# Kernel optimization log

Hardware: AMD Instinct MI355X
Metric: run time of the kernel (lower is better)

The kernel has to match this reference:

```python
import jax, jax.numpy as jnp
import numpy as np

B, S, D = 4, 2048, 1024
H = 16
HD = D // H
DFF = 4096
MAX_REL = 32
EPS = 1e-5


def _rms_norm(x, w):
    rms = jnp.sqrt(jnp.mean(x * x, axis=-1, keepdims=True) + EPS)
    return x / rms * w


def setup_inputs() -> dict:
    key = jax.random.key(0)
    ks = jax.random.split(key, 16)
    sc = 0.02
    d = {
        "x": jax.random.normal(ks[0], (B, S, D), dtype=jnp.float32),
        "g1": jnp.ones((D,), dtype=jnp.float32),
        "g2": jnp.ones((D,), dtype=jnp.float32),
        "wq": jax.random.normal(ks[1], (D, D), dtype=jnp.float32) * sc,
        "bq": jnp.zeros((D,), dtype=jnp.float32),
        "wk": jax.random.normal(ks[2], (D, D), dtype=jnp.float32) * sc,
        "bk": jnp.zeros((D,), dtype=jnp.float32),
        "wv": jax.random.normal(ks[3], (D, D), dtype=jnp.float32) * sc,
        "bv": jnp.zeros((D,), dtype=jnp.float32),
        "wo": jax.random.normal(ks[4], (D, D), dtype=jnp.float32) * sc,
        "bo": jnp.zeros((D,), dtype=jnp.float32),
        "rel_pos": jax.random.normal(ks[5], (H, 2 * MAX_REL + 1), dtype=jnp.float32),
        "w1": jax.random.normal(ks[6], (D, DFF), dtype=jnp.float32) * sc,
        "b1": jnp.zeros((DFF,), dtype=jnp.float32),
        "w2": jax.random.normal(ks[7], (DFF, D), dtype=jnp.float32) * sc,
        "b2": jnp.zeros((D,), dtype=jnp.float32),
    }
    return d


def reference(x, g1, g2, wq, bq, wk, bk, wv, bv, wo, bo, rel_pos, w1, b1, w2, b2):
    b, s, d = x.shape
    # --- multi-head attention with relative-position bias ---
    q = (x @ wq + bq).reshape(b, s, H, HD).transpose(0, 2, 1, 3)  # [B,H,S,HD]
    k = (x @ wk + bk).reshape(b, s, H, HD).transpose(0, 2, 1, 3)
    v = (x @ wv + bv).reshape(b, s, H, HD).transpose(0, 2, 1, 3)
    scores = jnp.einsum("bhqd,bhkd->bhqk", q, k) / jnp.sqrt(jnp.float32(HD))
    # relative position bias: gather from (H, 2*MAX_REL+1) table
    pos = jnp.arange(s)
    rel = pos[None, :] - pos[:, None]                # [S,S]
    idx = jnp.clip(rel, -MAX_REL, MAX_REL) + MAX_REL  # [S,S]
    bias = rel_pos[:, idx]                            # [H,S,S]
    scores = scores + bias[None]
    attn = jax.nn.softmax(scores, axis=-1)
    out = jnp.einsum("bhqk,bhkd->bhqd", attn, v)
    out = out.transpose(0, 2, 1, 3).reshape(b, s, d)
    attn_out = out @ wo + bo
    # residual + RMSNorm
    x = _rms_norm(attn_out + x, g1)
    # --- feed-forward (exact GELU) ---
    h = jax.nn.gelu(x @ w1 + b1, approximate=False)
    ff = h @ w2 + b2
    x = _rms_norm(ff + x, g2)
    return x
```

## Files before the change

kernel.cpp:

```cpp
#include <hip/hip_runtime.h>

#define B_ 4
#define S_ 2048
#define D_ 1024
#define H_ 16
#define HD_ 64
#define DFF_ 4096
#define MR_ 32
#define M_ (B_*S_)

typedef unsigned short u16;
typedef __attribute__((ext_vector_type(8))) short bf16x8;
typedef __attribute__((ext_vector_type(4))) float f32x4;

#define MFMA16 __builtin_amdgcn_mfma_f32_16x16x32_bf16
#define A_CONST 0.18033688011112f
#define LOG2E_ 1.44269504088896f

__device__ __forceinline__ u16 f2b(float f) {
  unsigned u = __builtin_bit_cast(unsigned, f);
  u = u + 0x7FFFu + ((u >> 16) & 1u);
  return (u16)(u >> 16);
}
__device__ __forceinline__ float b2f(u16 h) {
  unsigned u = ((unsigned)h) << 16;
  return __builtin_bit_cast(float, u);
}
__device__ __forceinline__ float exp2_fast(float x) {
  float r;
  asm("v_exp_f32 %0, %1" : "=v"(r) : "v"(x));
  return r;
}
__device__ __forceinline__ unsigned cvtpk(float lo, float hi) {
  unsigned r;
  asm("v_cvt_pk_bf16_f32 %0, %1, %2" : "=v"(r) : "v"(lo), "v"(hi));
  return r;
}
__device__ __forceinline__ int med3i(int a, int b, int c) {
  int r;
  asm("v_med3_i32 %0, %1, %2, %3" : "=v"(r) : "v"(a), "v"(b), "v"(c));
  return r;
}
__device__ __forceinline__ float gelu_t(float v) {
  float v2 = v * v;
  float z  = v * fmaf(v2, 0.1029394f, 2.3021171f);
  float e  = exp2_fast(z);
  float r;
  asm("v_rcp_f32 %0, %1" : "=v"(r) : "v"(e + 1.0f));
  return v - v * r;
}
__device__ __forceinline__ void gl_lds16(const void* g, void* l) {
  __builtin_amdgcn_global_load_lds(
      (const __attribute__((address_space(1))) void*)g,
      (__attribute__((address_space(3))) void*)l, 16, 0, 0);
}

#define SWZ(r) ((((((r)>>3)&1)<<2) ^ ((r)&7)) << 4)
#define SWZ64(r) ((((r)>>1)&3) << 4)

__global__ __launch_bounds__(256) void cvt_kernel(const float* __restrict__ in,
                                                  u16* __restrict__ out, int n4) {
  int i = blockIdx.x * 256 + threadIdx.x;
  if (i < n4) {
    float4 v = ((const float4*)in)[i];
    ushort4 o;
    o.x = f2b(v.x); o.y = f2b(v.y); o.z = f2b(v.z); o.w = f2b(v.w);
    ((ushort4*)out)[i] = o;
  }
}

__global__ __launch_bounds__(256) void wtrans_kernel(const float* __restrict__ in,
                                                     u16* __restrict__ out, int R, int C) {
  __shared__ float t[32][33];
  int c0 = blockIdx.x * 32, r0 = blockIdx.y * 32;
  int x = threadIdx.x, y = threadIdx.y;
#pragma unroll
  for (int i = 0; i < 4; ++i)
    t[y + i*8][x] = in[(long)(r0 + y + i*8) * C + c0 + x];
  __syncthreads();
#pragma unroll
  for (int i = 0; i < 4; ++i)
    out[(long)(c0 + y + i*8) * R + r0 + x] = f2b(t[x][y + i*8]);
}

__global__ __launch_bounds__(256) void vtrans_kernel(const u16* __restrict__ v,
                                                     u16* __restrict__ vT) {
  __shared__ u16 t[32][33];
  int bh = blockIdx.y; int b = bh >> 4, h = bh & 15;
  int s0 = (blockIdx.x >> 1) * 32;
  int d0 = (blockIdx.x & 1) * 32;
  int x = threadIdx.x, y = threadIdx.y;
#pragma unroll
  for (int i = 0; i < 4; ++i)
    t[y + i*8][x] = v[((long)(b*S_ + s0 + y + i*8)) * D_ + h*64 + d0 + x];
  __syncthreads();
#pragma unroll
  for (int i = 0; i < 4; ++i)
    vT[((long)((b*H_ + h)*HD_ + d0 + y + i*8)) * S_ + s0 + x] = t[x][y + i*8];
}

template<int EPI, int WN>
__global__ __launch_bounds__(512, 2) void gemm10(
    const u16* __restrict__ A, const u16* __restrict__ BT,
    const float* __restrict__ bias0, const float* __restrict__ bias1,
    const float* __restrict__ bias2,
    u16* __restrict__ C0, u16* __restrict__ C1, u16* __restrict__ C2,
    int Ndim, int Kdim)
{
  constexpr int BM = (WN == 4) ? 128 : 256;
  constexpr int BN = WN * 64;
  constexpr int SLOT = (BM + BN) * 64;
  __shared__ char lds[3 * SLOT];
  const int tid = threadIdx.x;
  const int w = tid >> 6, lane = tid & 63;
  const int lr = lane & 15, lg = lane >> 4;
  const int wm = w / WN, wn = w % WN;

  const int nbx = Ndim / BN;
  const int cpx = gridDim.x >> 3;
  const int bid = blockIdx.x;
  const int swzb = (bid & 7) * cpx + (bid >> 3);
  const long blockM = (long)(swzb / nbx) * BM;
  const long blockN = (long)(swzb % nbx) * BN;

  const int srow = tid >> 2;
  const int scol = ((tid & 3) * 16) ^ SWZ64(srow);
  const u16* Ag  = A  + (blockM + srow) * (long)Kdim + (scol >> 1);
  const u16* Ag2 = Ag + (long)128 * Kdim;
  const u16* Bg  = BT + (blockN + srow) * (long)Kdim + (scol >> 1);
  const u16* Bg2 = Bg + (long)128 * Kdim;

  auto STAGE = [&](int slot, long ko) {
    char* base = &lds[slot * SLOT];
    gl_lds16(Ag + ko, base + w * 1024);
    if constexpr (WN == 2) gl_lds16(Ag2 + ko, base + 8192 + w * 1024);
    gl_lds16(Bg + ko, base + BM * 64 + w * 1024);
    if constexpr (WN == 4) gl_lds16(Bg2 + ko, base + BM * 64 + 8192 + w * 1024);
  };

  const int rsw = (lg * 16) ^ SWZ64(lr);
  int offA[4], offB[4];
#pragma unroll
  for (int mf = 0; mf < 4; ++mf) offA[mf] = (wm*64 + mf*16 + lr) * 64 + rsw;
#pragma unroll
  for (int nf = 0; nf < 4; ++nf) offB[nf] = BM*64 + (wn*64 + nf*16 + lr) * 64 + rsw;

  f32x4 acc[4][4] = {};
  const int NS = Kdim >> 5;

  STAGE(0, 0);
  STAGE(1, 32);
  asm volatile("s_waitcnt vmcnt(3)" ::: "memory");
  __builtin_amdgcn_s_barrier();

  int sl = 0, sl2 = 2;
  for (int t = 0; t < NS; ++t) {
    const char* s = &lds[sl * SLOT];
    bf16x8 af[4], bfr[4];
#pragma unroll
    for (int mf = 0; mf < 4; ++mf) af[mf] = *(const bf16x8*)(s + offA[mf]);
#pragma unroll
    for (int nf = 0; nf < 4; ++nf) bfr[nf] = *(const bf16x8*)(s + offB[nf]);
    if (t + 2 < NS) {
      STAGE(sl2, (long)(t + 2) * 32);
      asm volatile("s_waitcnt vmcnt(3)" ::: "memory");
    } else if (t == NS - 2) {
      asm volatile("s_waitcnt vmcnt(0)" ::: "memory");
    }
    __builtin_amdgcn_s_barrier();
    __builtin_amdgcn_s_setprio(1);
#pragma unroll
    for (int mf = 0; mf < 4; ++mf)
#pragma unroll
      for (int nf = 0; nf < 4; ++nf)
        acc[mf][nf] = MFMA16(bfr[nf], af[mf], acc[mf][nf], 0, 0, 0);
    __builtin_amdgcn_s_setprio(0);
    __builtin_amdgcn_s_barrier();
    sl  = (sl  == 2) ? 0 : sl  + 1;
    sl2 = (sl2 == 2) ? 0 : sl2 + 1;
  }

  const float* bsel = bias0;
  u16* osel = C0;
  long nstride = Ndim;
  long ncol0 = blockN;
  if (EPI == 3) {
    int mat = (int)(blockN >> 10);
    bsel = mat == 0 ? bias0 : (mat == 1 ? bias1 : bias2);
    osel = mat == 0 ? C0 : (mat == 1 ? C1 : C2);
    nstride = 1024;
    ncol0 = blockN & 1023;
  }
  constexpr int RB = BN * 2;
  char* const et = &lds[0];
#pragma unroll
  for (int mf = 0; mf < 4; ++mf) {
    const int row = wm*64 + mf*16 + lr;
#pragma unroll
    for (int nf = 0; nf < 4; ++nf) {
      const int colu = wn*64 + nf*16 + lg*4;
      float4 bv = *(const float4*)&bsel[ncol0 + colu];
      float v0 = acc[mf][nf][0] + bv.x;
      float v1 = acc[mf][nf][1] + bv.y;
      float v2 = acc[mf][nf][2] + bv.z;
      float v3 = acc[mf][nf][3] + bv.w;
      if (EPI == 2) {
        v0 = gelu_t(v0); v1 = gelu_t(v1); v2 = gelu_t(v2); v3 = gelu_t(v3);
      }
      ushort4 st;
      st.x = f2b(v0); st.y = f2b(v1); st.z = f2b(v2); st.w = f2b(v3);
      *(ushort4*)(et + row*RB + ((colu*2) ^ ((row & 7) << 4))) = st;
    }
  }
  __syncthreads();
  constexpr int CHR  = RB / 16;
  constexpr int ITER = BM * CHR / 512;
#pragma unroll
  for (int i = 0; i < ITER; ++i) {
    const int idx = i*512 + tid;
    const int row = idx / CHR;
    const int cb  = (idx % CHR) * 16;
    uint4 val = *(const uint4*)(et + row*RB + (cb ^ ((row & 7) << 4)));
    *(uint4*)&osel[(blockM + row) * nstride + ncol0 + (cb >> 1)] = val;
  }
}

__device__ __forceinline__ void packp(const float* p, bf16x8* pfo) {
#pragma unroll
  for (int ks = 0; ks < 2; ++ks) {
    uint4 uu;
    uu.x = cvtpk(p[ks*4+0], p[ks*4+1]);
    uu.y = cvtpk(p[ks*4+2], p[ks*4+3]);
    uu.z = cvtpk(p[(ks+2)*4+0], p[(ks+2)*4+1]);
    uu.w = cvtpk(p[(ks+2)*4+2], p[(ks+2)*4+3]);
    pfo[ks] = __builtin_bit_cast(bf16x8, uu);
  }
}

__device__ __forceinline__ void sm_uni(const f32x4* s, float bu, bf16x8* pfo) {
  float p[16];
#pragma unroll
  for (int ni = 0; ni < 4; ++ni)
#pragma unroll
    for (int j = 0; j < 4; ++j)
      p[ni*4+j] = exp2_fast(fmaf(s[ni][j], A_CONST, bu));
  packp(p, pfo);
}

__device__ __forceinline__ void sm_slow(const f32x4* s, const float* relb,
                                        int rbase, bf16x8* pfo) {
  float p[16];
#pragma unroll
  for (int ni = 0; ni < 4; ++ni) {
    const int koff = (ni&1)*32 + (ni>>1)*4;
#pragma unroll
    for (int j = 0; j < 4; ++j) {
      int idx = med3i(rbase + koff + j + MR_, 0, 2*MR_);
      p[ni*4+j] = exp2_fast(fmaf(s[ni][j], A_CONST, relb[idx]));
    }
  }
  packp(p, pfo);
}

__global__ __launch_bounds__(256, 4) void attn5_kernel(
    const u16* __restrict__ q, const u16* __restrict__ k,
    const u16* __restrict__ vT, const float* __restrict__ rel_pos,
    u16* __restrict__ ao)
{
  __shared__ u16 KB[2][4096];
  __shared__ u16 VB[2][4096];
  __shared__ float relb[2*MR_ + 1];

  const int tid = threadIdx.x;
  const int w = tid >> 6, lane = tid & 63;
  const int lr = lane & 15, lg = lane >> 4;
  const int qt = blockIdx.x, bh = blockIdx.y;
  const int b = bh >> 4, h = bh & 15;
  const int q0 = qt * 128;
  const int qq = q0 + w*32;

  if (tid < 2*MR_ + 1) relb[tid] = rel_pos[h * (2*MR_ + 1) + tid] * LOG2E_;

  const int srow0 = w*8 + (lane >> 3);
  const int srow1 = 32 + srow0;
  const int scb   = (lane & 7) * 16;
  const int col0  = scb ^ SWZ(srow0);
  const int col1  = scb ^ SWZ(srow1);

  const long qkbase = ((long)(b*S_)) * D_ + h*64;
  const long vbase  = ((long)((b*H_ + h) * HD_)) * S_;

  {
    const u16* qg = q + qkbase + (long)q0 * D_;
#pragma unroll
    for (int c = 0; c < 4; ++c) {
      int row = c*32 + srow0;
      int colc = scb ^ SWZ(row);
      gl_lds16(qg + (long)row*D_ + (colc >> 1), &KB[0][0] + (c*32 + w*8)*64);
    }
  }
  __syncthreads();
  bf16x8 qf[4];
#pragma unroll
  for (int qi = 0; qi < 2; ++qi)
#pragma unroll
    for (int ks = 0; ks < 2; ++ks) {
      int row = w*32 + qi*16 + lr;
      qf[qi*2+ks] = *(const bf16x8*)((const char*)&KB[0][0] + row*128 + ((ks*64 + lg*16) ^ SWZ(row)));
    }
  const float bHI = relb[2*MR_];
  const float bLO = relb[0];
  __syncthreads();

  int offK0[4], offV0[4];
#pragma unroll
  for (int ni = 0; ni < 4; ++ni) {
    int kr = (ni&1)*32 + (lr>>2)*8 + (ni>>1)*4 + (lr&3);
    int vr = ni*16 + lr;
    offK0[ni] = kr*128 + ((lg*16) ^ SWZ(kr));
    offV0[ni] = vr*128 + ((lg*16) ^ SWZ(vr));
  }

  const u16* kp0 = k  + qkbase + (long)srow0*D_ + (col0 >> 1);
  const u16* kp1 = k  + qkbase + (long)srow1*D_ + (col1 >> 1);
  const u16* vp0 = vT + vbase  + (long)srow0*S_ + (col0 >> 1);
  const u16* vp1 = vT + vbase  + (long)srow1*S_ + (col1 >> 1);
  u16* kb_w0 = &KB[0][(w*8)*64];
  u16* kb_w1 = &KB[0][(32 + w*8)*64];
  u16* vb_w0 = &VB[0][(w*8)*64];
  u16* vb_w1 = &VB[0][(32 + w*8)*64];

  bf16x8 onesf;
#pragma unroll
  for (int i = 0; i < 8; ++i) onesf[i] = (short)0x3F80;

  f32x4 acco[2][4] = {};
  f32x4 accl[2] = {};

  gl_lds16(kp0, kb_w0);
  gl_lds16(kp1, kb_w1);
  gl_lds16(vp0, vb_w0);
  gl_lds16(vp1, vb_w1);

  const long kstep = (long)64 * D_;
  const int NT = S_ / 64;
  for (int t = 0; t < NT; ++t) {
    const int cur = t & 1;
    __syncthreads();
    if (t + 1 < NT) {
      int bufo = (cur ^ 1) * 4096;
      gl_lds16(kp0 + (long)(t+1)*kstep, kb_w0 + bufo);
      gl_lds16(kp1 + (long)(t+1)*kstep, kb_w1 + bufo);
      gl_lds16(vp0 + (t+1)*64, vb_w0 + bufo);
      gl_lds16(vp1 + (t+1)*64, vb_w1 + bufo);
    }
    const char* Kb = (const char*)&KB[cur][0];
    const char* Vb = (const char*)&VB[cur][0];
    const int k0 = t * 64;

    f32x4 s0[4] = {}, s1[4] = {};
#pragma unroll
    for (int ks = 0; ks < 2; ++ks)
#pragma unroll
      for (int ni = 0; ni < 4; ++ni) {
        bf16x8 kf = *(const bf16x8*)(Kb + (offK0[ni] ^ (ks*64)));
        s0[ni] = MFMA16(kf, qf[ks],   s0[ni], 0, 0, 0);
        s1[ni] = MFMA16(kf, qf[2+ks], s1[ni], 0, 0, 0);
      }

    bf16x8 pf0[2], pf1[2];
    bool hi_u = (k0 - (qq + 31)) >= MR_;
    bool lo_u = (qq - (k0 + 63)) >= MR_;
    if (hi_u || lo_u) {
      float bu = hi_u ? bHI : bLO;
      sm_uni(s0, bu, pf0);
      sm_uni(s1, bu, pf1);
    } else {
      int rb0 = k0 + lg*8 - (qq + lr);
      sm_slow(s0, relb, rb0,      pf0);
      sm_slow(s1, relb, rb0 - 16, pf1);
    }

#pragma unroll
    for (int ks = 0; ks < 2; ++ks) {
#pragma unroll
      for (int ni = 0; ni < 4; ++ni) {
        bf16x8 vf = *(const bf16x8*)(Vb + (offV0[ni] ^ (ks*64)));
        acco[0][ni] = MFMA16(vf, pf0[ks], acco[0][ni], 0, 0, 0);
        acco[1][ni] = MFMA16(vf, pf1[ks], acco[1][ni], 0, 0, 0);
      }
      accl[0] = MFMA16(onesf, pf0[ks], accl[0], 0, 0, 0);
      accl[1] = MFMA16(onesf, pf1[ks], accl[1], 0, 0, 0);
    }
  }

#pragma unroll
  for (int qi = 0; qi < 2; ++qi) {
    float inv = 1.0f / accl[qi][0];
    long orow = ((long)(b*S_ + qq + qi*16 + lr)) * D_ + h*64;
#pragma unroll
    for (int ni = 0; ni < 4; ++ni) {
      ushort4 ov;
      ov.x = f2b(acco[qi][ni][0] * inv);
      ov.y = f2b(acco[qi][ni][1] * inv);
      ov.z = f2b(acco[qi][ni][2] * inv);
      ov.w = f2b(acco[qi][ni][3] * inv);
      *(ushort4*)(ao + orow + ni*16 + lg*4) = ov;
    }
  }
}

template<int ABF, int BBF>
__global__ __launch_bounds__(256) void rmsnorm_kernel(
    const void* __restrict__ a, const void* __restrict__ b,
    const float* __restrict__ g, float* __restrict__ outf,
    u16* __restrict__ outb)
{
  long row = blockIdx.x;
  int tid = threadIdx.x;
  float ya[4], yb[4], y[4];
  if (ABF) {
    ushort4 av = ((const ushort4*)a)[row*256 + tid];
    ya[0] = b2f(av.x); ya[1] = b2f(av.y); ya[2] = b2f(av.z); ya[3] = b2f(av.w);
  } else {
    float4 av = ((const float4*)a)[row*256 + tid];
    ya[0] = av.x; ya[1] = av.y; ya[2] = av.z; ya[3] = av.w;
  }
  if (BBF) {
    ushort4 bv = ((const ushort4*)b)[row*256 + tid];
    yb[0] = b2f(bv.x); yb[1] = b2f(bv.y); yb[2] = b2f(bv.z); yb[3] = b2f(bv.w);
  } else {
    float4 bv = ((const float4*)b)[row*256 + tid];
    yb[0] = bv.x; yb[1] = bv.y; yb[2] = bv.z; yb[3] = bv.w;
  }
  float ss = 0.f;
#pragma unroll
  for (int i = 0; i < 4; ++i) { y[i] = ya[i] + yb[i]; ss += y[i]*y[i]; }
#pragma unroll
  for (int m = 1; m < 64; m <<= 1) ss += __shfl_xor(ss, m);
  __shared__ float red[4];
  int w = tid >> 6, lane = tid & 63;
  if (lane == 0) red[w] = ss;
  __syncthreads();
  ss = red[0] + red[1] + red[2] + red[3];
  float rinv = rsqrtf(ss * (1.0f / D_) + 1e-5f);
  float4 gv = ((const float4*)g)[tid];
  float o[4] = { y[0]*rinv*gv.x, y[1]*rinv*gv.y, y[2]*rinv*gv.z, y[3]*rinv*gv.w };
  if (outf) {
    float4 of = { o[0], o[1], o[2], o[3] };
    ((float4*)outf)[row*256 + tid] = of;
  }
  if (outb) {
    ushort4 ob;
    ob.x = f2b(o[0]); ob.y = f2b(o[1]); ob.z = f2b(o[2]); ob.w = f2b(o[3]);
    ((ushort4*)outb)[row*256 + tid] = ob;
  }
}

extern "C" void kernel_launch(void* const* d_in, const int* in_sizes, int n_in,
                              void* d_out, int out_size, void* d_ws, size_t ws_size,
                              hipStream_t stream) {
  const float* x   = (const float*)d_in[0];
  const float* g1  = (const float*)d_in[1];
  const float* g2  = (const float*)d_in[2];
  const float* wq  = (const float*)d_in[3];
  const float* bq  = (const float*)d_in[4];
  const float* wk  = (const float*)d_in[5];
  const float* bk  = (const float*)d_in[6];
  const float* wv  = (const float*)d_in[7];
  const float* bv  = (const float*)d_in[8];
  const float* wo  = (const float*)d_in[9];
  const float* bo  = (const float*)d_in[10];
  const float* rel = (const float*)d_in[11];
  const float* w1  = (const float*)d_in[12];
  const float* b1  = (const float*)d_in[13];
  const float* w2  = (const float*)d_in[14];
  const float* b2  = (const float*)d_in[15];
  float* out = (float*)d_out;

  char* ws = (char*)d_ws;
  const size_t MB = 1024ull * 1024ull;
  u16* xb   = (u16*)(ws + 0);
  u16* wqT  = (u16*)(ws + 16*MB);
  u16* wkT  = (u16*)(ws + 18*MB);
  u16* wvT  = (u16*)(ws + 20*MB);
  u16* woT  = (u16*)(ws + 22*MB);
  u16* w1T  = (u16*)(ws + 24*MB);
  u16* w2T  = (u16*)(ws + 32*MB);
  u16* qb   = (u16*)(ws + 40*MB);
  u16* kb   = (u16*)(ws + 56*MB);
  u16* vb   = (u16*)(ws + 72*MB);
  u16* vTb  = (u16*)(ws + 88*MB);
  u16* aob  = (u16*)(ws + 104*MB);
  u16* prjb = (u16*)(ws + 120*MB);
  u16* x1b  = (u16*)(ws + 136*MB);
  u16* hb   = (u16*)(ws + 40*MB);
  u16* ffb  = (u16*)(ws + 120*MB);
  (void)ws_size; (void)in_sizes; (void)n_in; (void)out_size;

  dim3 tb(32, 8);

  cvt_kernel<<<M_*D_/4/256, 256, 0, stream>>>(x, xb, M_*D_/4);
  wtrans_kernel<<<dim3(D_/32,   D_/32),   tb, 0, stream>>>(wq, wqT, D_,   D_);
  wtrans_kernel<<<dim3(D_/32,   D_/32),   tb, 0, stream>>>(wk, wkT, D_,   D_);
  wtrans_kernel<<<dim3(D_/32,   D_/32),   tb, 0, stream>>>(wv, wvT, D_,   D_);
  wtrans_kernel<<<dim3(D_/32,   D_/32),   tb, 0, stream>>>(wo, woT, D_,   D_);
  wtrans_kernel<<<dim3(DFF_/32, D_/32),   tb, 0, stream>>>(w1, w1T, D_,   DFF_);
  wtrans_kernel<<<dim3(D_/32,   DFF_/32), tb, 0, stream>>>(w2, w2T, DFF_, D_);

  gemm10<3,4><<<(3072/256)*(M_/128), 512, 0, stream>>>(
      xb, wqT, bq, bk, bv, qb, kb, vb, 3072, D_);

  vtrans_kernel<<<dim3((S_/32)*(HD_/32), B_*H_), tb, 0, stream>>>(vb, vTb);

  attn5_kernel<<<dim3(S_/128, B_*H_), 256, 0, stream>>>(qb, kb, vTb, rel, aob);

  gemm10<0,2><<<(D_/128)*(M_/256), 512, 0, stream>>>(
      aob, woT, bo, nullptr, nullptr, prjb, nullptr, nullptr, D_, D_);

  rmsnorm_kernel<1,1><<<M_, 256, 0, stream>>>(prjb, xb, g1, nullptr, x1b);

  gemm10<2,4><<<(DFF_/256)*(M_/128), 512, 0, stream>>>(
      x1b, w1T, b1, nullptr, nullptr, hb, nullptr, nullptr, DFF_, D_);

  gemm10<0,2><<<(D_/128)*(M_/256), 512, 0, stream>>>(
      hb, w2T, b2, nullptr, nullptr, ffb, nullptr, nullptr, D_, DFF_);

  rmsnorm_kernel<1,1><<<M_, 256, 0, stream>>>(ffb, x1b, g2, out, nullptr);
}
```

Before: 412.9 us.

## Add 128x128 triple-buffered GEMM for N=1024 projections; shuffle rel-pos bias in attention

Adds a new 256-thread GEMM kernel with 128x128 tiles, a three-slot LDS ring, prefetch two steps ahead and an XCD-style block swizzle. It is used for the output projection and the second FFN GEMM (N=1024), which previously ran the 512-thread 256x128 tile kernel. The aim is more blocks in flight and better latency hiding on these narrow-N GEMMs. Separately, the attention kernel now keeps the relative-position table in registers, one entry per lane, and reads it with wave shuffles instead of a shared-memory array. Index 64 is outside the 64 lanes, so it is handled with a select on the high bias value.

```diff
diff --git a/kernel.cpp b/kernel.cpp
--- a/kernel.cpp
+++ b/kernel.cpp
@@ -225,6 +225,114 @@
   }
 }
 
+template<int EPI>
+__global__ __launch_bounds__(256, 3) void gemm12(
+    const u16* __restrict__ A, const u16* __restrict__ BT,
+    const float* __restrict__ bias0, u16* __restrict__ C0,
+    int Ndim, int Kdim)
+{
+  constexpr int SLOT = 16384;
+  __shared__ char lds[3 * SLOT];
+  const int tid = threadIdx.x;
+  const int w = tid >> 6, lane = tid & 63;
+  const int lr = lane & 15, lg = lane >> 4;
+  const int wm = w >> 1, wn = w & 1;
+
+  const int nbx = Ndim >> 7;
+  const int cpx = gridDim.x >> 3;
+  const int bid = blockIdx.x;
+  const int swzb = (bid & 7) * cpx + (bid >> 3);
+  const long blockM = (long)(swzb / nbx) * 128;
+  const long blockN = (long)(swzb % nbx) * 128;
+
+  const int srow = tid >> 2;
+  const int scol = ((tid & 3) * 16) ^ SWZ64(srow);
+  const u16* Ag  = A  + (blockM + srow) * (long)Kdim + (scol >> 1);
+  const u16* Ag2 = Ag + (long)64 * Kdim;
+  const u16* Bg  = BT + (blockN + srow) * (long)Kdim + (scol >> 1);
+  const u16* Bg2 = Bg + (long)64 * Kdim;
+
+  auto STAGE = [&](int slot, long ko) {
+    char* base = &lds[slot * SLOT];
+    gl_lds16(Ag  + ko, base +         w * 1024);
+    gl_lds16(Ag2 + ko, base + 4096  + w * 1024);
+    gl_lds16(Bg  + ko, base + 8192  + w * 1024);
+    gl_lds16(Bg2 + ko, base + 12288 + w * 1024);
+  };
+
+  const int rsw = (lg * 16) ^ SWZ64(lr);
+  int offA[4], offB[4];
+#pragma unroll
+  for (int mf = 0; mf < 4; ++mf) offA[mf] = (wm*64 + mf*16 + lr) * 64 + rsw;
+#pragma unroll
+  for (int nf = 0; nf < 4; ++nf) offB[nf] = 8192 + (wn*64 + nf*16 + lr) * 64 + rsw;
+
+  f32x4 acc[4][4] = {};
+  const int NS = Kdim >> 5;
+
+  STAGE(0, 0);
+  STAGE(1, 32);
+  asm volatile("s_waitcnt vmcnt(4)" ::: "memory");
+  __builtin_amdgcn_s_barrier();
+
+  int sl = 0, sl2 = 2;
+  for (int t = 0; t < NS; ++t) {
+    const char* s = &lds[sl * SLOT];
+    bf16x8 af[4], bfr[4];
+#pragma unroll
+    for (int mf = 0; mf < 4; ++mf) af[mf] = *(const bf16x8*)(s + offA[mf]);
+#pragma unroll
+    for (int nf = 0; nf < 4; ++nf) bfr[nf] = *(const bf16x8*)(s + offB[nf]);
+    if (t + 2 < NS) {
+      STAGE(sl2, (long)(t + 2) * 32);
+      asm volatile("s_waitcnt vmcnt(4)" ::: "memory");
+    } else if (t == NS - 2) {
+      asm volatile("s_waitcnt vmcnt(0)" ::: "memory");
+    }
+    __builtin_amdgcn_s_barrier();
+    __builtin_amdgcn_s_setprio(1);
+#pragma unroll
+    for (int mf = 0; mf < 4; ++mf)
+#pragma unroll
+      for (int nf = 0; nf < 4; ++nf)
+        acc[mf][nf] = MFMA16(bfr[nf], af[mf], acc[mf][nf], 0, 0, 0);
+    __builtin_amdgcn_s_setprio(0);
+    __builtin_amdgcn_s_barrier();
+    sl  = (sl  == 2) ? 0 : sl  + 1;
+    sl2 = (sl2 == 2) ? 0 : sl2 + 1;
+  }
+
+  char* const et = &lds[0];
+#pragma unroll
+  for (int mf = 0; mf < 4; ++mf) {
+    const int row = wm*64 + mf*16 + lr;
+#pragma unroll
+    for (int nf = 0; nf < 4; ++nf) {
+      const int colu = wn*64 + nf*16 + lg*4;
+      float4 bv = *(const float4*)&bias0[blockN + colu];
+      float v0 = acc[mf][nf][0] + bv.x;
+      float v1 = acc[mf][nf][1] + bv.y;
+      float v2 = acc[mf][nf][2] + bv.z;
+      float v3 = acc[mf][nf][3] + bv.w;
+      if (EPI == 2) {
+        v0 = gelu_t(v0); v1 = gelu_t(v1); v2 = gelu_t(v2); v3 = gelu_t(v3);
+      }
+      ushort4 st;
+      st.x = f2b(v0); st.y = f2b(v1); st.z = f2b(v2); st.w = f2b(v3);
+      *(ushort4*)(et + row*256 + ((colu*2) ^ ((row & 7) << 4))) = st;
+    }
+  }
+  __syncthreads();
+#pragma unroll
+  for (int i = 0; i < 8; ++i) {
+    const int idx = i*256 + tid;
+    const int row = idx >> 4;
+    const int cb  = (idx & 15) * 16;
+    uint4 val = *(const uint4*)(et + row*256 + (cb ^ ((row & 7) << 4)));
+    *(uint4*)&C0[(blockM + row) * (long)Ndim + blockN + (cb >> 1)] = val;
+  }
+}
+
 __device__ __forceinline__ void packp(const float* p, bf16x8* pfo) {
 #pragma unroll
   for (int ks = 0; ks < 2; ++ks) {
@@ -247,7 +355,7 @@
   packp(p, pfo);
 }
 
-__device__ __forceinline__ void sm_slow(const f32x4* s, const float* relb,
+__device__ __forceinline__ void sm_slow(const f32x4* s, float rp, float bHI,
                                         int rbase, bf16x8* pfo) {
   float p[16];
 #pragma unroll
@@ -256,20 +364,21 @@
 #pragma unroll
     for (int j = 0; j < 4; ++j) {
       int idx = med3i(rbase + koff + j + MR_, 0, 2*MR_);
-      p[ni*4+j] = exp2_fast(fmaf(s[ni][j], A_CONST, relb[idx]));
+      float bb = __shfl(rp, idx);
+      bb = (idx >= 64) ? bHI : bb;
+      p[ni*4+j] = exp2_fast(fmaf(s[ni][j], A_CONST, bb));
     }
   }
   packp(p, pfo);
 }
 
-__global__ __launch_bounds__(256, 4) void attn5_kernel(
+__global__ __launch_bounds__(256, 4) void attn6_kernel(
     const u16* __restrict__ q, const u16* __restrict__ k,
     const u16* __restrict__ vT, const float* __restrict__ rel_pos,
     u16* __restrict__ ao)
 {
   __shared__ u16 KB[2][4096];
   __shared__ u16 VB[2][4096];
-  __shared__ float relb[2*MR_ + 1];
 
   const int tid = threadIdx.x;
   const int w = tid >> 6, lane = tid & 63;
@@ -279,7 +388,9 @@
   const int q0 = qt * 128;
   const int qq = q0 + w*32;
 
-  if (tid < 2*MR_ + 1) relb[tid] = rel_pos[h * (2*MR_ + 1) + tid] * LOG2E_;
+  const float rp  = rel_pos[h*(2*MR_+1) + lane] * LOG2E_;
+  const float bHI = rel_pos[h*(2*MR_+1) + 2*MR_] * LOG2E_;
+  const float bLO = rel_pos[h*(2*MR_+1)] * LOG2E_;
 
   const int srow0 = w*8 + (lane >> 3);
   const int srow1 = 32 + srow0;
@@ -308,8 +419,6 @@
       int row = w*32 + qi*16 + lr;
       qf[qi*2+ks] = *(const bf16x8*)((const char*)&KB[0][0] + row*128 + ((ks*64 + lg*16) ^ SWZ(row)));
     }
-  const float bHI = relb[2*MR_];
-  const float bLO = relb[0];
   __syncthreads();
 
   int offK0[4], offV0[4];
@@ -377,8 +486,8 @@
       sm_uni(s1, bu, pf1);
     } else {
       int rb0 = k0 + lg*8 - (qq + lr);
-      sm_slow(s0, relb, rb0,      pf0);
-      sm_slow(s1, relb, rb0 - 16, pf1);
+      sm_slow(s0, rp, bHI, rb0,      pf0);
+      sm_slow(s1, rp, bHI, rb0 - 16, pf1);
     }
 
 #pragma unroll
@@ -513,18 +622,16 @@
 
   vtrans_kernel<<<dim3((S_/32)*(HD_/32), B_*H_), tb, 0, stream>>>(vb, vTb);
 
-  attn5_kernel<<<dim3(S_/128, B_*H_), 256, 0, stream>>>(qb, kb, vTb, rel, aob);
-
-  gemm10<0,2><<<(D_/128)*(M_/256), 512, 0, stream>>>(
-      aob, woT, bo, nullptr, nullptr, prjb, nullptr, nullptr, D_, D_);
+  attn6_kernel<<<dim3(S_/128, B_*H_), 256, 0, stream>>>(qb, kb, vTb, rel, aob);
+
+  gemm12<0><<<(D_/128)*(M_/128), 256, 0, stream>>>(aob, woT, bo, prjb, D_, D_);
 
   rmsnorm_kernel<1,1><<<M_, 256, 0, stream>>>(prjb, xb, g1, nullptr, x1b);
 
   gemm10<2,4><<<(DFF_/256)*(M_/128), 512, 0, stream>>>(
       x1b, w1T, b1, nullptr, nullptr, hb, nullptr, nullptr, DFF_, D_);
 
-  gemm10<0,2><<<(D_/128)*(M_/256), 512, 0, stream>>>(
-      hb, w2T, b2, nullptr, nullptr, ffb, nullptr, nullptr, D_, DFF_);
+  gemm12<0><<<(D_/128)*(M_/128), 256, 0, stream>>>(hb, w2T, b2, ffb, D_, DFF_);
 
   rmsnorm_kernel<1,1><<<M_, 256, 0, stream>>>(ffb, x1b, g2, out, nullptr);
 }
```

Result: slower. 422.7 us (+2.4%).
